# Optimization experiments

Measured on AMD Instinct MI355X. Metric: run time of the kernel, lower is better.

Reference implementation:

```python
import jax, jax.numpy as jnp
import numpy as np

EPS = 1e-6

def setup_inputs() -> dict:
    key = jax.random.key(0)
    k1, k2, k3, k4, k5 = jax.random.split(key, 5)
    B, Lq, Lk, D, Dc = 8, 1024, 8192, 256, 128
    q = jax.random.normal(k1, (B, Lq, D), dtype=jnp.float32)
    k_q = jax.random.randint(k2, (B, Lk, Dc), 0, 16, dtype=jnp.int32)  # 4-bit codes
    k_scale = jax.random.uniform(k3, (B, 1, Dc), dtype=jnp.float32)
    k_zero = jax.random.uniform(k4, (B, 1, Dc), dtype=jnp.float32) * 15.0
    W_up = jax.random.normal(k5, (D, Dc), dtype=jnp.float32) / np.sqrt(Dc)
    return {"q": q, "k_q": k_q, "k_scale": k_scale, "k_zero": k_zero, "W_up": W_up}

def reference(q, k_q, k_scale, k_zero, W_up):
    # int4 dequantization: (B, Lk, Dc)
    k_c = k_scale * (k_q.astype(jnp.float32) - k_zero)
    # low-rank decompress (nn.Linear(d_compressed, d_model, bias=False)): k = k_c @ W_up.T -> (B, Lk, D)
    k = jnp.einsum('blc,dc->bld', k_c, W_up)
    # squared norms (raw values used in diff, clamped values used in denominator)
    q_sq = jnp.sum(q * q, axis=-1)  # (B, Lq)
    k_sq = jnp.sum(k * k, axis=-1)  # (B, Lk)
    q_norm_sq = jnp.minimum(q_sq, 1.0 - EPS)
    k_norm_sq = jnp.minimum(k_sq, 1.0 - EPS)
    # ||q_i - k_j||^2 via expansion (same math as materializing the diff tensor)
    qk = jnp.einsum('bqd,bkd->bqk', q, k)  # (B, Lq, Lk)
    diff_norm_sq = jnp.maximum(q_sq[:, :, None] + k_sq[:, None, :] - 2.0 * qk, 0.0)
    denom = (1.0 - q_norm_sq)[:, :, None] * (1.0 - k_norm_sq)[:, None, :] + EPS
    dist = jnp.arccosh(1.0 + 2.0 * diff_norm_sq / denom)  # (B, Lq, Lk)
    return dist
```

## Files before the change

### kernel.cpp

```cpp
#include <hip/hip_runtime.h>
#include <hip/hip_bf16.h>

#define B_   8
#define LQ   1024
#define LK   8192
#define D_   256
#define DC   128
#define EPSF 1e-6f

typedef __attribute__((ext_vector_type(8))) short short8;
typedef __attribute__((ext_vector_type(4))) float floatx4;

static __device__ __forceinline__ floatx4 mfma16(short8 a, short8 b, floatx4 c) {
    return __builtin_amdgcn_mfma_f32_16x16x32_bf16(a, b, c, 0, 0, 0);
}
static __device__ __forceinline__ float fast_rcp(float x)  { return __builtin_amdgcn_rcpf(x); }
static __device__ __forceinline__ float fast_sqrt(float x) { return __builtin_amdgcn_sqrtf(x); }
static __device__ __forceinline__ float fast_ln(float x)   { return 0.69314718056f * __builtin_amdgcn_logf(x); }

__global__ __launch_bounds__(256) void k_G(const float* __restrict__ W,
                                           __hip_bfloat16* __restrict__ G,
                                           __hip_bfloat16* __restrict__ Wt) {
    __shared__ float red[128];
    int c1 = blockIdx.x;
    int t = threadIdx.x, c2 = t & 127, h = t >> 7;
    int d0 = h * 128;
    float a0 = 0.f, a1 = 0.f, a2 = 0.f, a3 = 0.f;
#pragma unroll 4
    for (int d = 0; d < 128; d += 4) {
        a0 += W[(size_t)(d0 + d + 0) * DC + c1] * W[(size_t)(d0 + d + 0) * DC + c2];
        a1 += W[(size_t)(d0 + d + 1) * DC + c1] * W[(size_t)(d0 + d + 1) * DC + c2];
        a2 += W[(size_t)(d0 + d + 2) * DC + c1] * W[(size_t)(d0 + d + 2) * DC + c2];
        a3 += W[(size_t)(d0 + d + 3) * DC + c1] * W[(size_t)(d0 + d + 3) * DC + c2];
    }
    float s = (a0 + a1) + (a2 + a3);
    if (h) red[c2] = s;
    Wt[(size_t)c1 * D_ + t] = __float2bfloat16(W[(size_t)t * DC + c1]);
    __syncthreads();
    if (!h) G[c1 * DC + c2] = __float2bfloat16(s + red[c2]);
}

__global__ __launch_bounds__(256) void k_qproj(const float* __restrict__ q,
                                               const __hip_bfloat16* __restrict__ Wt,
                                               __hip_bfloat16* __restrict__ qproj,
                                               float* __restrict__ q_sq) {
    __shared__ __hip_bfloat16 sA[64 * 72];
    __shared__ __hip_bfloat16 sB[128 * 72];
    int t = threadIdx.x, lane = t & 63, w = t >> 6;
    int quad = lane >> 4, li = lane & 15;
    int row0 = blockIdx.x * 64;

    float psum[4] = {0.f, 0.f, 0.f, 0.f};
    floatx4 acc[8];
#pragma unroll
    for (int nt = 0; nt < 8; ++nt) acc[nt] = (floatx4){0.f, 0.f, 0.f, 0.f};

    for (int kc4 = 0; kc4 < 4; ++kc4) {
#pragma unroll
        for (int it = 0; it < 4; ++it) {
            int idx = it * 256 + t;
            int r = idx >> 4, pos = idx & 15;
            float4 v = *(const float4*)(q + (size_t)(row0 + r) * D_ + kc4 * 64 + pos * 4);
            psum[it] += v.x * v.x + v.y * v.y + v.z * v.z + v.w * v.w;
            __hip_bfloat16* dst = &sA[r * 72 + pos * 4];
            dst[0] = __float2bfloat16(v.x); dst[1] = __float2bfloat16(v.y);
            dst[2] = __float2bfloat16(v.z); dst[3] = __float2bfloat16(v.w);
        }
#pragma unroll
        for (int it = 0; it < 4; ++it) {
            int e = it * 256 + t;
            int c = e >> 3, ch = e & 7;
            *(uint4*)&sB[c * 72 + ch * 8] =
                *(const uint4*)(Wt + (size_t)c * D_ + kc4 * 64 + ch * 8);
        }
        __syncthreads();
        short8 af[2];
#pragma unroll
        for (int ks = 0; ks < 2; ++ks)
            af[ks] = *(const short8*)&sA[(w * 16 + li) * 72 + ks * 32 + quad * 8];
#pragma unroll
        for (int nt = 0; nt < 8; ++nt)
#pragma unroll
            for (int ks = 0; ks < 2; ++ks) {
                short8 bf = *(const short8*)&sB[(nt * 16 + li) * 72 + ks * 32 + quad * 8];
                acc[nt] = mfma16(af[ks], bf, acc[nt]);
            }
        __syncthreads();
    }
#pragma unroll
    for (int nt = 0; nt < 8; ++nt)
#pragma unroll
        for (int r = 0; r < 4; ++r) {
            int row = w * 16 + quad * 4 + r;
            qproj[(size_t)(row0 + row) * DC + nt * 16 + li] = __float2bfloat16(acc[nt][r]);
        }
#pragma unroll
    for (int it = 0; it < 4; ++it) {
        float s = psum[it];
        s += __shfl_xor(s, 1); s += __shfl_xor(s, 2);
        s += __shfl_xor(s, 4); s += __shfl_xor(s, 8);
        if (li == 0) q_sq[row0 + it * 16 + w * 4 + quad] = s;
    }
}

__global__ __launch_bounds__(256) void k_dq_ksq(const int* __restrict__ kq,
                                                const float* __restrict__ kscale,
                                                const float* __restrict__ kzero,
                                                const __hip_bfloat16* __restrict__ G,
                                                __hip_bfloat16* __restrict__ kc,
                                                float* __restrict__ k_sq) {
    __shared__ __hip_bfloat16 sK[64 * 132];
    int t = threadIdx.x, lane = t & 63, w = t >> 6;
    int quad = lane >> 4, li = lane & 15;
    int b = blockIdx.x >> 7, l0 = (blockIdx.x & 127) * 64;

    const int4* codes = (const int4*)(kq + ((size_t)b * LK + l0) * DC);
    int col = (t & 31) * 4;
    float4 sc = *(const float4*)(kscale + b * DC + col);
    float4 zp = *(const float4*)(kzero + b * DC + col);
    __hip_bfloat16* kco = kc + ((size_t)b * LK + l0) * DC;
#pragma unroll
    for (int it = 0; it < 8; ++it) {
        int idx = it * 256 + t;
        int r = idx >> 5;
        int4 c4 = codes[idx];
        __hip_bfloat16 tmp[4];
        tmp[0] = __float2bfloat16(sc.x * ((float)c4.x - zp.x));
        tmp[1] = __float2bfloat16(sc.y * ((float)c4.y - zp.y));
        tmp[2] = __float2bfloat16(sc.z * ((float)c4.z - zp.z));
        tmp[3] = __float2bfloat16(sc.w * ((float)c4.w - zp.w));
        *(uint2*)&sK[r * 132 + col] = *(const uint2*)tmp;
        *(uint2*)(kco + idx * 4)    = *(const uint2*)tmp;
    }
    __syncthreads();

    short8 af[4];
#pragma unroll
    for (int ks = 0; ks < 4; ++ks)
        af[ks] = *(const short8*)&sK[(w * 16 + li) * 132 + ks * 32 + quad * 8];
    float s4[4] = {0.f, 0.f, 0.f, 0.f};
#pragma unroll
    for (int nt = 0; nt < 8; ++nt) {
        floatx4 a0 = (floatx4){0.f, 0.f, 0.f, 0.f};
#pragma unroll
        for (int ks = 0; ks < 4; ++ks) {
            short8 bf = *(const short8*)(G + (size_t)(nt * 16 + li) * DC + ks * 32 + quad * 8);
            a0 = mfma16(af[ks], bf, a0);
        }
        int c2 = nt * 16 + li;
#pragma unroll
        for (int r = 0; r < 4; ++r)
            s4[r] += a0[r] * __bfloat162float(sK[(w * 16 + quad * 4 + r) * 132 + c2]);
    }
#pragma unroll
    for (int r = 0; r < 4; ++r) {
        float v = s4[r];
        v += __shfl_xor(v, 1); v += __shfl_xor(v, 2);
        v += __shfl_xor(v, 4); v += __shfl_xor(v, 8);
        if (li == 0)
            k_sq[(size_t)b * LK + l0 + w * 16 + quad * 4 + r] = v;
    }
}

__global__ __launch_bounds__(256) void k_main(const __hip_bfloat16* __restrict__ qproj,
                                              const __hip_bfloat16* __restrict__ kc,
                                              const float* __restrict__ q_sq,
                                              const float* __restrict__ k_sq,
                                              float* __restrict__ out) {
    __shared__ __align__(16) char smem[128 * 72 * 2 * 2];
    __hip_bfloat16* sA = (__hip_bfloat16*)smem;
    __hip_bfloat16* sB = sA + 128 * 72;
    float* sO = (float*)smem;

    int t = threadIdx.x, lane = t & 63, w = t >> 6;
    int quad = lane >> 4, li = lane & 15;
    int wm = w >> 1, wn = w & 1;
    int n0 = blockIdx.x * 128, m0 = blockIdx.y * 128, b = blockIdx.z;
    const uint4* Ag = (const uint4*)(qproj + ((size_t)b * LQ + m0) * DC);
    const uint4* Bg = (const uint4*)(kc   + ((size_t)b * LK + n0) * DC);
    uint4* dA = (uint4*)sA; uint4* dB = (uint4*)sB;

    floatx4 acc[4][4];
#pragma unroll
    for (int i = 0; i < 4; ++i)
#pragma unroll
        for (int j = 0; j < 4; ++j)
            acc[i][j] = (floatx4){0.f, 0.f, 0.f, 0.f};

    int r_ = t >> 3, ch_ = t & 7;
    uint4 ra[4], rb[4];
#pragma unroll
    for (int it = 0; it < 4; ++it) {
        ra[it] = Ag[(it * 32 + r_) * 16 + ch_];
        rb[it] = Bg[(it * 32 + r_) * 16 + ch_];
    }
#pragma unroll
    for (int it = 0; it < 4; ++it) {
        dA[(it * 32 + r_) * 9 + ch_] = ra[it];
        dB[(it * 32 + r_) * 9 + ch_] = rb[it];
    }
    __syncthreads();
#pragma unroll
    for (int it = 0; it < 4; ++it) {
        ra[it] = Ag[(it * 32 + r_) * 16 + 8 + ch_];
        rb[it] = Bg[(it * 32 + r_) * 16 + 8 + ch_];
    }
#pragma unroll
    for (int ks = 0; ks < 2; ++ks) {
        short8 qf[4], kf[4];
#pragma unroll
        for (int i = 0; i < 4; ++i) {
            qf[i] = *(const short8*)&sA[(wm * 64 + i * 16 + li) * 72 + ks * 32 + quad * 8];
            kf[i] = *(const short8*)&sB[(wn * 64 + i * 16 + li) * 72 + ks * 32 + quad * 8];
        }
#pragma unroll
        for (int i = 0; i < 4; ++i)
#pragma unroll
            for (int j = 0; j < 4; ++j)
                acc[i][j] = mfma16(kf[j], qf[i], acc[i][j]);
    }
    __syncthreads();
#pragma unroll
    for (int it = 0; it < 4; ++it) {
        dA[(it * 32 + r_) * 9 + ch_] = ra[it];
        dB[(it * 32 + r_) * 9 + ch_] = rb[it];
    }
    __syncthreads();
#pragma unroll
    for (int ks = 0; ks < 2; ++ks) {
        short8 qf[4], kf[4];
#pragma unroll
        for (int i = 0; i < 4; ++i) {
            qf[i] = *(const short8*)&sA[(wm * 64 + i * 16 + li) * 72 + ks * 32 + quad * 8];
            kf[i] = *(const short8*)&sB[(wn * 64 + i * 16 + li) * 72 + ks * 32 + quad * 8];
        }
#pragma unroll
        for (int i = 0; i < 4; ++i)
#pragma unroll
            for (int j = 0; j < 4; ++j)
                acc[i][j] = mfma16(kf[j], qf[i], acc[i][j]);
    }

    int orow_t = t >> 4;
    int ocol4  = (t & 15) * 4;
    float qsA[8], omqA[8];
#pragma unroll
    for (int qq = 0; qq < 8; ++qq) {
        qsA[qq]  = q_sq[(size_t)b * LQ + m0 + qq * 16 + orow_t];
        omqA[qq] = 1.f - fminf(qsA[qq], 1.f - EPSF);
    }
#pragma unroll
    for (int p = 0; p < 2; ++p) {
        __syncthreads();
#pragma unroll
        for (int jj = 0; jj < 2; ++jj) {
            int c = wn * 32 + jj * 16 + quad * 4;
#pragma unroll
            for (int i = 0; i < 4; ++i) {
                int m = wm * 64 + i * 16 + li;
                *(floatx4*)&sO[m * 68 + c] = acc[i][p * 2 + jj];
            }
        }
        __syncthreads();
        int nbase = (ocol4 >> 5) * 64 + p * 32 + (ocol4 & 31);
        floatx4 ks4 = *(const floatx4*)(k_sq + (size_t)b * LK + n0 + nbase);
        floatx4 kn;
#pragma unroll
        for (int r = 0; r < 4; ++r)
            kn[r] = 1.f - fminf(ks4[r], 1.f - EPSF);
#pragma unroll
        for (int qq = 0; qq < 8; ++qq) {
            int row = qq * 16 + orow_t;
            floatx4 v = *(const floatx4*)&sO[row * 68 + ocol4];
            float qs = qsA[qq], omq = omqA[qq];
            floatx4 o;
#pragma unroll
            for (int r = 0; r < 4; ++r) {
                float diff  = fmaxf(qs + ks4[r] - 2.f * v[r], 0.f);
                float delta = 2.f * diff * fast_rcp(omq * kn[r] + EPSF);
                float sq    = fast_sqrt(delta * (delta + 2.f));
                o[r] = fast_ln(1.f + delta + sq);
            }
            __builtin_nontemporal_store(
                o, (floatx4*)(out + ((size_t)b * LQ + m0 + row) * (size_t)LK + n0 + nbase));
        }
    }
}

extern "C" void kernel_launch(void* const* d_in, const int* in_sizes, int n_in,
                              void* d_out, int out_size, void* d_ws, size_t ws_size,
                              hipStream_t stream) {
    const float* q      = (const float*)d_in[0];
    const int*   kq     = (const int*)d_in[1];
    const float* kscale = (const float*)d_in[2];
    const float* kzero  = (const float*)d_in[3];
    const float* W      = (const float*)d_in[4];
    float* out = (float*)d_out;

    char* ws = (char*)d_ws;
    __hip_bfloat16* qproj = (__hip_bfloat16*)(ws);
    __hip_bfloat16* kc    = (__hip_bfloat16*)(ws + 2097152);
    __hip_bfloat16* G     = (__hip_bfloat16*)(ws + 18874368);
    float*          q_sq  = (float*)(ws + 18907136);
    float*          k_sq  = (float*)(ws + 18939904);
    __hip_bfloat16* Wt    = kc;

    k_G     <<<128, 256, 0, stream>>>(W, G, Wt);
    k_qproj <<<128, 256, 0, stream>>>(q, Wt, qproj, q_sq);
    k_dq_ksq<<<1024, 256, 0, stream>>>(kq, kscale, kzero, G, kc, k_sq);
    dim3 grid(LK / 128, LQ / 128, B_);
    k_main  <<<grid, 256, 0, stream>>>(qproj, kc, q_sq, k_sq, out);
}
```

Baseline: 386.3 us.

## Widen small prep kernels and remap main-kernel block order across batches

k_G now runs 512 threads per block and splits the reduction four ways. k_qproj now uses 32-row tiles so twice as many blocks launch, with warps split across N. k_main now uses a flattened 1D grid whose block index puts batch in the fastest-varying bits, then m tile, then n tile. The intent is to raise occupancy in the prep kernels and change the order tiles are scheduled, which may affect L2 reuse of the qproj and kc tiles.

```diff
diff --git a/kernel.cpp b/kernel.cpp
--- a/kernel.cpp
+++ b/kernel.cpp
@@ -18,46 +18,48 @@
 static __device__ __forceinline__ float fast_sqrt(float x) { return __builtin_amdgcn_sqrtf(x); }
 static __device__ __forceinline__ float fast_ln(float x)   { return 0.69314718056f * __builtin_amdgcn_logf(x); }
 
-__global__ __launch_bounds__(256) void k_G(const float* __restrict__ W,
+__global__ __launch_bounds__(512) void k_G(const float* __restrict__ W,
                                            __hip_bfloat16* __restrict__ G,
                                            __hip_bfloat16* __restrict__ Wt) {
-    __shared__ float red[128];
+    __shared__ float red[512];
     int c1 = blockIdx.x;
     int t = threadIdx.x, c2 = t & 127, h = t >> 7;
-    int d0 = h * 128;
+    int d0 = h * 64;
     float a0 = 0.f, a1 = 0.f, a2 = 0.f, a3 = 0.f;
 #pragma unroll 4
-    for (int d = 0; d < 128; d += 4) {
+    for (int d = 0; d < 64; d += 4) {
         a0 += W[(size_t)(d0 + d + 0) * DC + c1] * W[(size_t)(d0 + d + 0) * DC + c2];
         a1 += W[(size_t)(d0 + d + 1) * DC + c1] * W[(size_t)(d0 + d + 1) * DC + c2];
         a2 += W[(size_t)(d0 + d + 2) * DC + c1] * W[(size_t)(d0 + d + 2) * DC + c2];
         a3 += W[(size_t)(d0 + d + 3) * DC + c1] * W[(size_t)(d0 + d + 3) * DC + c2];
     }
-    float s = (a0 + a1) + (a2 + a3);
-    if (h) red[c2] = s;
-    Wt[(size_t)c1 * D_ + t] = __float2bfloat16(W[(size_t)t * DC + c1]);
-    __syncthreads();
-    if (!h) G[c1 * DC + c2] = __float2bfloat16(s + red[c2]);
+    red[t] = (a0 + a1) + (a2 + a3);
+    if (t < 256) Wt[(size_t)c1 * D_ + t] = __float2bfloat16(W[(size_t)t * DC + c1]);
+    __syncthreads();
+    if (h == 0)
+        G[c1 * DC + c2] =
+            __float2bfloat16(red[c2] + red[128 + c2] + red[256 + c2] + red[384 + c2]);
 }
 
 __global__ __launch_bounds__(256) void k_qproj(const float* __restrict__ q,
                                                const __hip_bfloat16* __restrict__ Wt,
                                                __hip_bfloat16* __restrict__ qproj,
                                                float* __restrict__ q_sq) {
-    __shared__ __hip_bfloat16 sA[64 * 72];
+    __shared__ __hip_bfloat16 sA[32 * 72];
     __shared__ __hip_bfloat16 sB[128 * 72];
     int t = threadIdx.x, lane = t & 63, w = t >> 6;
     int quad = lane >> 4, li = lane & 15;
-    int row0 = blockIdx.x * 64;
-
-    float psum[4] = {0.f, 0.f, 0.f, 0.f};
-    floatx4 acc[8];
-#pragma unroll
-    for (int nt = 0; nt < 8; ++nt) acc[nt] = (floatx4){0.f, 0.f, 0.f, 0.f};
+    int wm = w >> 1, wn = w & 1;
+    int row0 = blockIdx.x * 32;
+
+    float psum[2] = {0.f, 0.f};
+    floatx4 acc[4];
+#pragma unroll
+    for (int nt = 0; nt < 4; ++nt) acc[nt] = (floatx4){0.f, 0.f, 0.f, 0.f};
 
     for (int kc4 = 0; kc4 < 4; ++kc4) {
 #pragma unroll
-        for (int it = 0; it < 4; ++it) {
+        for (int it = 0; it < 2; ++it) {
             int idx = it * 256 + t;
             int r = idx >> 4, pos = idx & 15;
             float4 v = *(const float4*)(q + (size_t)(row0 + r) * D_ + kc4 * 64 + pos * 4);
@@ -77,25 +79,26 @@
         short8 af[2];
 #pragma unroll
         for (int ks = 0; ks < 2; ++ks)
-            af[ks] = *(const short8*)&sA[(w * 16 + li) * 72 + ks * 32 + quad * 8];
-#pragma unroll
-        for (int nt = 0; nt < 8; ++nt)
+            af[ks] = *(const short8*)&sA[(wm * 16 + li) * 72 + ks * 32 + quad * 8];
+#pragma unroll
+        for (int nt = 0; nt < 4; ++nt)
 #pragma unroll
             for (int ks = 0; ks < 2; ++ks) {
-                short8 bf = *(const short8*)&sB[(nt * 16 + li) * 72 + ks * 32 + quad * 8];
+                short8 bf = *(const short8*)&sB[((wn * 4 + nt) * 16 + li) * 72 + ks * 32 + quad * 8];
                 acc[nt] = mfma16(af[ks], bf, acc[nt]);
             }
         __syncthreads();
     }
 #pragma unroll
-    for (int nt = 0; nt < 8; ++nt)
+    for (int nt = 0; nt < 4; ++nt)
 #pragma unroll
         for (int r = 0; r < 4; ++r) {
-            int row = w * 16 + quad * 4 + r;
-            qproj[(size_t)(row0 + row) * DC + nt * 16 + li] = __float2bfloat16(acc[nt][r]);
-        }
-#pragma unroll
-    for (int it = 0; it < 4; ++it) {
+            int row = wm * 16 + quad * 4 + r;
+            qproj[(size_t)(row0 + row) * DC + (wn * 4 + nt) * 16 + li] =
+                __float2bfloat16(acc[nt][r]);
+        }
+#pragma unroll
+    for (int it = 0; it < 2; ++it) {
         float s = psum[it];
         s += __shfl_xor(s, 1); s += __shfl_xor(s, 2);
         s += __shfl_xor(s, 4); s += __shfl_xor(s, 8);
@@ -175,7 +178,11 @@
     int t = threadIdx.x, lane = t & 63, w = t >> 6;
     int quad = lane >> 4, li = lane & 15;
     int wm = w >> 1, wn = w & 1;
-    int n0 = blockIdx.x * 128, m0 = blockIdx.y * 128, b = blockIdx.z;
+    int bid = blockIdx.x;
+    int b   = bid & 7;
+    int rem = bid >> 3;
+    int m0  = (rem & 7) << 7;
+    int n0  = (rem >> 3) << 7;
     const uint4* Ag = (const uint4*)(qproj + ((size_t)b * LQ + m0) * DC);
     const uint4* Bg = (const uint4*)(kc   + ((size_t)b * LK + n0) * DC);
     uint4* dA = (uint4*)sA; uint4* dB = (uint4*)sB;
@@ -305,9 +312,8 @@
     float*          k_sq  = (float*)(ws + 18939904);
     __hip_bfloat16* Wt    = kc;
 
-    k_G     <<<128, 256, 0, stream>>>(W, G, Wt);
-    k_qproj <<<128, 256, 0, stream>>>(q, Wt, qproj, q_sq);
+    k_G     <<<128, 512, 0, stream>>>(W, G, Wt);
+    k_qproj <<<256, 256, 0, stream>>>(q, Wt, qproj, q_sq);
     k_dq_ksq<<<1024, 256, 0, stream>>>(kq, kscale, kzero, G, kc, k_sq);
-    dim3 grid(LK / 128, LQ / 128, B_);
-    k_main  <<<grid, 256, 0, stream>>>(qproj, kc, q_sq, k_sq, out);
-}
+    k_main  <<<4096, 256, 0, stream>>>(qproj, kc, q_sq, k_sq, out);
+}
```

Result: no change. 388.9 us (+0.7%).
